# Optimization experiments

Hardware: AMD Instinct MI355X
Metric: run time of the kernel (lower is better)

Reference implementation:

```python
import jax, jax.numpy as jnp
import numpy as np

B, G1, S, GS, D, T, H = 64, 128, 32, 16, 384, 10, 6
HD = D // H
SCALE = HD ** -0.5
GELU = lambda v: jax.nn.gelu(v, approximate=False)


def layer_norm(v, g, b, eps=1e-5):
    m = jnp.mean(v, -1, keepdims=True)
    s = jnp.mean((v - m) ** 2, -1, keepdims=True)
    return (v - m) * jax.lax.rsqrt(s + eps) * g + b


def mha(xn, qkv_w, proj_w, proj_b):
    Bc, N, C = xn.shape
    qkv = (xn @ qkv_w.T).reshape(Bc, N, 3, H, HD)
    qkv = jnp.transpose(qkv, (2, 0, 3, 1, 4))  # [3,B,H,N,hd]
    q, k, v = qkv[0], qkv[1], qkv[2]
    attn = jax.nn.softmax(jnp.einsum('bhnd,bhmd->bhnm', q, k) * SCALE, axis=-1)
    o = jnp.einsum('bhnm,bhmd->bhnd', attn, v)
    o = jnp.transpose(o, (0, 2, 1, 3)).reshape(Bc, N, C)
    return o @ proj_w.T + proj_b, attn


def propagate(xyz1, xyz2, points1, points2, de_neighbors):
    # squared pairwise distances [B,N,S]
    d = jnp.sum((xyz1[:, :, None, :] - xyz2[:, None, :, :]) ** 2, -1)
    order = jnp.argsort(d, axis=-1)[..., :de_neighbors]
    dists = jnp.take_along_axis(d, order, axis=-1)
    w = 1.0 / (dists + 1e-8)
    w = w / jnp.sum(w, -1, keepdims=True)
    gathered = jax.vmap(lambda p, i: p[i])(points2, order)  # [B,N,de,Dp]
    interp = jnp.sum(gathered * w[..., None], axis=2)
    return points1 + 0.3 * interp


def setup_inputs() -> dict:
    key = jax.random.key(0)
    ks = iter(jax.random.split(key, 64))
    rn = lambda sh, sc=1.0: jax.random.normal(next(ks), sh, jnp.float32) * sc
    w = 0.02
    inp = dict(
        x=rn((B, G1 + 1, D)),
        mask=jnp.zeros((B, G1, G1), jnp.float32),
        center1=rn((B, G1, 3)),
        center2=rn((B, S, 3)),
        neighborhood=rn((B, S, GS, 3)),
        idx=jax.random.randint(next(ks), (B * S * GS,), 0, B * (G1 + T)),
        center_idx=jax.random.randint(next(ks), (B * S,), 0, B * (G1 + T)),
        group_size=GS,
        layer_id=3,
        ln1_g=jnp.ones((D,)), ln1_b=jnp.zeros((D,)),
        ln2_g=jnp.ones((D,)), ln2_b=jnp.zeros((D,)),
        qkv_w=rn((3 * D, D), w), proj_w=rn((D, D), w), proj_b=jnp.zeros((D,)),
        fc1_w=rn((4 * D, D), w), fc1_b=jnp.zeros((4 * D,)),
        fc2_w=rn((D, 4 * D), w), fc2_b=jnp.zeros((D,)),
        ad_down_w=rn((16, D), w), ad_down_b=jnp.zeros((16,)),
        ad_up_w=rn((D, 16), w), ad_up_b=jnp.zeros((D,)),
        ad1_down_w=rn((16, D), w), ad1_down_b=jnp.zeros((16,)),
        ad1_up_w=rn((D, 16), w), ad1_up_b=jnp.zeros((D,)),
        prompt_emb=rn((T, D), w),
        bn_g=jnp.ones((D,)), bn_b=jnp.zeros((D,)),
        bn_mean=jnp.zeros((D,)), bn_var=jnp.ones((D,)),
        qkv1_w=rn((3 * D, D), w), proj1_w=rn((D, D), w), proj1_b=jnp.zeros((D,)),
        ln3_g=jnp.ones((D,)), ln3_b=jnp.zeros((D,)),
    )
    return inp


def block_forward(x, mask, center1, center2, neighborhood, idx, center_idx,
                  group_size, layer_id,
                  ln1_g, ln1_b, ln2_g, ln2_b, qkv_w, proj_w, proj_b,
                  fc1_w, fc1_b, fc2_w, fc2_b,
                  ad_down_w, ad_down_b, ad_up_w, ad_up_b,
                  ad1_down_w, ad1_down_b, ad1_up_w, ad1_up_b,
                  prompt_emb, bn_g, bn_b, bn_mean, bn_var,
                  qkv1_w, proj1_w, proj1_b, ln3_g, ln3_b):
    Bc = x.shape[0]
    # mask padding (built but unused by Attention, matching the source)
    # layer_id <= 5 branch (layer_id=3)
    prompt = jnp.broadcast_to(prompt_emb[None], (Bc, T, D))  # dropout off (eval)
    x = jnp.concatenate([x[:, :1], prompt, x[:, 1:]], axis=1)  # [B, 1+T+G1, D]
    x_fn, attn_weight = mha(layer_norm(x, ln1_g, ln1_b), qkv_w, proj_w, proj_b)
    x = x_fn + x
    xn2 = layer_norm(x, ln2_g, ln2_b)
    x_fn = GELU(xn2 @ fc1_w.T + fc1_b) @ fc2_w.T + fc2_b
    # AdapterSuper_f: bottleneck down-GELU-up (no internal residual)
    ad = GELU(x_fn @ ad_down_w.T + ad_down_b) @ ad_up_w.T + ad_up_b
    x = 0.7 * ad + x_fn + x
    prompt = x[:, 1:T + 1]
    x = jnp.concatenate([x[:, :1], x[:, T + 1:]], axis=1)  # [B, 1+G1, D]
    cls_x = x[:, 0]
    x = x[:, 1:]  # [B, G1, D]
    G = G1 + T
    prompt_x = jnp.concatenate([prompt, x], axis=1).reshape(Bc * G, D)
    x_neigh = prompt_x[idx].reshape(Bc * S, group_size, D)
    x_centers = prompt_x[center_idx].reshape(Bc, S, D)
    _ = neighborhood / (jnp.std(neighborhood) + 1e-5)  # dead in source
    # local attention over each neighborhood group
    xn3 = layer_norm(x_neigh, ln3_g, ln3_b)
    attn1_out, _a = mha(xn3, qkv1_w, proj1_w, proj1_b)
    x_neigh = attn1_out + x_neigh
    # pooling: max over group, then eval BatchNorm1d + GELU over channel dim
    lc = jnp.max(x_neigh.reshape(Bc, S, group_size, D), axis=2)  # [B,S,D]
    lc = (lc - bn_mean) * jax.lax.rsqrt(bn_var + 1e-5) * bn_g + bn_b
    lc = GELU(lc)
    vis_x = lc + 0.3 * x_centers
    x = propagate(center1, center2, x, vis_x, S)
    x = jnp.concatenate([cls_x[:, None], prompt, x], axis=1)  # [B, 1+T+G1, D]
    # AdapterSuper: bottleneck with internal residual
    x = GELU(x @ ad1_down_w.T + ad1_down_b) @ ad1_up_w.T + ad1_up_b + x
    x = jnp.concatenate([x[:, :1], x[:, T + 1:]], axis=1)  # [B, 1+G1, D]
    return x, attn_weight


def reference(x, mask, center1, center2, neighborhood, idx, center_idx,
              group_size, layer_id,
              ln1_g, ln1_b, ln2_g, ln2_b, qkv_w, proj_w, proj_b,
              fc1_w, fc1_b, fc2_w, fc2_b,
              ad_down_w, ad_down_b, ad_up_w, ad_up_b,
              ad1_down_w, ad1_down_b, ad1_up_w, ad1_up_b,
              prompt_emb, bn_g, bn_b, bn_mean, bn_var,
              qkv1_w, proj1_w, proj1_b, ln3_g, ln3_b):
    return block_forward(x, mask, center1, center2, neighborhood, idx, center_idx,
                         group_size, layer_id,
                         ln1_g, ln1_b, ln2_g, ln2_b, qkv_w, proj_w, proj_b,
                         fc1_w, fc1_b, fc2_w, fc2_b,
                         ad_down_w, ad_down_b, ad_up_w, ad_up_b,
                         ad1_down_w, ad1_down_b, ad1_up_w, ad1_up_b,
                         prompt_emb, bn_g, bn_b, bn_mean, bn_var,
                         qkv1_w, proj1_w, proj1_b, ln3_g, ln3_b)
```

## Files before the change

kernel.cpp:

```cpp
#include <hip/hip_runtime.h>
#include <hip/hip_bf16.h>

typedef __hip_bfloat16 bf16;
typedef __attribute__((ext_vector_type(8))) short short8;
typedef __attribute__((ext_vector_type(4))) float f32x4;

#define DEV static __device__ __forceinline__

DEV float b2f(bf16 v) { return __bfloat162float(v); }
DEV bf16 f2b(float v) { return __float2bfloat16(v); }
DEV unsigned short f2bu(float v) { return __builtin_bit_cast(unsigned short, __float2bfloat16(v)); }
DEV float u2f(unsigned short u) { return __uint_as_float(((unsigned int)u) << 16); }
DEV float gelu(float x) { return 0.5f * x * (1.0f + erff(x * 0.70710678118654752f)); }

#define BB 64
#define NT 139
#define DD 384
#define TT 10
#define HH 6
#define GG 138
#define M1 8896
#define MG 8832
#define NGRP 2048
#define SCALE 0.125f

#define XC_OFF   0UL
#define VIS_OFF  13664256UL
#define XNB_OFF  16809984UL
#define XFN_OFF  23642112UL
#define T16_OFF  37306368UL
#define BIG1_OFF 37875712UL
#define BIG2_OFF 58372096UL
#define ATT_OFF  XNB_OFF
#define WB_OFF   85700608UL

#define WB_QKV   0
#define WB_PROJ  442368
#define WB_FC1   589824
#define WB_FC2   1179648
#define WB_QKV1  1769472
#define WB_PROJ1 2211840
#define WB_TOTAL 2359296

#define OUT_X 3170304

DEV float4 ld4(const float* p) { return *(const float4*)p; }
DEV float4 ld4(const bf16* p) {
    ushort4 u = *(const ushort4*)p;
    return make_float4(u2f(u.x), u2f(u.y), u2f(u.z), u2f(u.w));
}
DEV void stc(float* p, float v) { *p = v; }
DEV void stc(bf16* p, float v) { *p = f2b(v); }

__global__ __launch_bounds__(256) void k_wconv(const float* __restrict__ w0, const float* __restrict__ w1,
                                               const float* __restrict__ w2, const float* __restrict__ w3,
                                               const float* __restrict__ w4, const float* __restrict__ w5,
                                               bf16* __restrict__ dst) {
    int i4 = (blockIdx.x * 256 + threadIdx.x) * 4;
    if (i4 >= WB_TOTAL) return;
    const float* s; int off;
    if (i4 < WB_PROJ)       { s = w0; off = WB_QKV; }
    else if (i4 < WB_FC1)   { s = w1; off = WB_PROJ; }
    else if (i4 < WB_FC2)   { s = w2; off = WB_FC1; }
    else if (i4 < WB_QKV1)  { s = w3; off = WB_FC2; }
    else if (i4 < WB_PROJ1) { s = w4; off = WB_QKV1; }
    else                    { s = w5; off = WB_PROJ1; }
    float4 v = *(const float4*)(s + (i4 - off));
    ushort4 u;
    u.x = f2bu(v.x); u.y = f2bu(v.y); u.z = f2bu(v.z); u.w = f2bu(v.w);
    *(ushort4*)((unsigned short*)dst + i4) = u;
}

__global__ __launch_bounds__(256) void k_build_xc(const float* __restrict__ x,
                                                  const float* __restrict__ pe,
                                                  float* __restrict__ xc) {
    int i = blockIdx.x * 256 + threadIdx.x;
    if (i >= M1 * DD) return;
    int d = i % DD, r = i / DD, n = r % NT, b = r / NT;
    float v;
    if (n == 0)        v = x[(b * 129) * DD + d];
    else if (n <= TT)  v = pe[(n - 1) * DD + d];
    else               v = x[(b * 129 + n - TT) * DD + d];
    xc[i] = v;
}

__global__ __launch_bounds__(128) void k_layernorm(const float* __restrict__ src, bf16* __restrict__ dst,
                                                   const float* __restrict__ g, const float* __restrict__ bta,
                                                   int mode) {
    int r = blockIdx.x;
    int srow = r;
    if (mode) srow = (r / GG) * NT + 1 + (r % GG);
    const float* p = src + (size_t)srow * DD;
    int t = threadIdx.x;
    float v0 = p[t], v1 = p[t + 128], v2 = p[t + 256];
    __shared__ float red[4];
    float s = v0 + v1 + v2;
    for (int off = 32; off; off >>= 1) s += __shfl_down(s, off, 64);
    if ((t & 63) == 0) red[t >> 6] = s;
    __syncthreads();
    float mean = (red[0] + red[1]) * (1.0f / 384.0f);
    float d0 = v0 - mean, d1 = v1 - mean, d2 = v2 - mean;
    float s2 = d0 * d0 + d1 * d1 + d2 * d2;
    for (int off = 32; off; off >>= 1) s2 += __shfl_down(s2, off, 64);
    if ((t & 63) == 0) red[2 + (t >> 6)] = s2;
    __syncthreads();
    float rstd = rsqrtf((red[2] + red[3]) * (1.0f / 384.0f) + 1e-5f);
    bf16* q = dst + (size_t)r * DD;
    q[t]       = f2b(d0 * rstd * g[t]       + bta[t]);
    q[t + 128] = f2b(d1 * rstd * g[t + 128] + bta[t + 128]);
    q[t + 256] = f2b(d2 * rstd * g[t + 256] + bta[t + 256]);
}

template <typename TC>
__global__ __launch_bounds__(256) void mf_gemm(const bf16* __restrict__ A, const bf16* __restrict__ W,
                                               const float* __restrict__ bias, const float* __restrict__ res,
                                               TC* __restrict__ C, int M, int N, int K, int act) {
    __shared__ bf16 As[64][72];
    __shared__ bf16 Ws[64][72];
    int t = threadIdx.x;
    int m0 = blockIdx.y * 64, n0 = blockIdx.x * 64;
    int lane = t & 63, wv = t >> 6;
    int wm = (wv >> 1) * 32, wn = (wv & 1) * 32;
    int fr = lane & 15, fq = lane >> 4;
    int sr = t >> 2, sc = (t & 3) * 16;
    const bf16* pa = A + (size_t)(m0 + sr) * K + sc;
    const bf16* pw = W + (size_t)(n0 + sr) * K + sc;
    uint4 ra0 = *(const uint4*)pa;
    uint4 ra1 = *(const uint4*)(pa + 8);
    uint4 rw0 = *(const uint4*)pw;
    uint4 rw1 = *(const uint4*)(pw + 8);
    f32x4 acc[2][2] = {};
    int k0 = 0;
    for (;;) {
        *(uint4*)&As[sr][sc] = ra0; *(uint4*)&As[sr][sc + 8] = ra1;
        *(uint4*)&Ws[sr][sc] = rw0; *(uint4*)&Ws[sr][sc + 8] = rw1;
        __syncthreads();
        k0 += 64;
        bool more = (k0 < K);
        if (more) {
            ra0 = *(const uint4*)(pa + k0); ra1 = *(const uint4*)(pa + k0 + 8);
            rw0 = *(const uint4*)(pw + k0); rw1 = *(const uint4*)(pw + k0 + 8);
        }
#pragma unroll
        for (int ks = 0; ks < 2; ++ks) {
            short8 a0 = *(const short8*)&As[wm + fr][ks * 32 + fq * 8];
            short8 a1 = *(const short8*)&As[wm + 16 + fr][ks * 32 + fq * 8];
            short8 b0 = *(const short8*)&Ws[wn + fr][ks * 32 + fq * 8];
            short8 b1 = *(const short8*)&Ws[wn + 16 + fr][ks * 32 + fq * 8];
            acc[0][0] = __builtin_amdgcn_mfma_f32_16x16x32_bf16(a0, b0, acc[0][0], 0, 0, 0);
            acc[0][1] = __builtin_amdgcn_mfma_f32_16x16x32_bf16(a0, b1, acc[0][1], 0, 0, 0);
            acc[1][0] = __builtin_amdgcn_mfma_f32_16x16x32_bf16(a1, b0, acc[1][0], 0, 0, 0);
            acc[1][1] = __builtin_amdgcn_mfma_f32_16x16x32_bf16(a1, b1, acc[1][1], 0, 0, 0);
        }
        if (!more) break;
        __syncthreads();
    }
#pragma unroll
    for (int i = 0; i < 2; ++i) {
#pragma unroll
        for (int r = 0; r < 4; ++r) {
            int row = m0 + wm + i * 16 + fq * 4 + r;
            size_t ro = (size_t)row * N;
#pragma unroll
            for (int j = 0; j < 2; ++j) {
                int col = n0 + wn + j * 16 + fr;
                float c = acc[i][j][r];
                if (bias) c += bias[col];
                if (act == 1) c = gelu(c);
                if (res) c += res[ro + col];
                stc(&C[ro + col], c);
            }
        }
    }
}

#define BM 64
#define BN 64
#define BKK 16
template <typename TA, typename TC>
__global__ __launch_bounds__(256) void k_gemm(const TA* __restrict__ A, const float* __restrict__ W,
                                              const float* __restrict__ bias, const float* __restrict__ res,
                                              TC* __restrict__ C, int M, int N, int K, int act) {
    __shared__ float As[BKK][BM + 4];
    __shared__ float Wsm[BKK][BN + 4];
    int t = threadIdx.x;
    int tx = t & 15, ty = t >> 4;
    int m0 = blockIdx.y * BM, n0 = blockIdx.x * BN;
    int lr = t >> 2;
    int lk = (t & 3) * 4;
    float acc[4][4] = {};
    for (int k0 = 0; k0 < K; k0 += BKK) {
        float4 av = ld4(A + (size_t)(m0 + lr) * K + k0 + lk);
        As[lk + 0][lr] = av.x; As[lk + 1][lr] = av.y;
        As[lk + 2][lr] = av.z; As[lk + 3][lr] = av.w;
        int wrr = n0 + lr;
        float4 wv = make_float4(0.f, 0.f, 0.f, 0.f);
        if (wrr < N) wv = ld4(W + (size_t)wrr * K + k0 + lk);
        Wsm[lk + 0][lr] = wv.x; Wsm[lk + 1][lr] = wv.y;
        Wsm[lk + 2][lr] = wv.z; Wsm[lk + 3][lr] = wv.w;
        __syncthreads();
#pragma unroll
        for (int k = 0; k < BKK; ++k) {
            float a0 = As[k][ty * 4 + 0], a1 = As[k][ty * 4 + 1];
            float a2 = As[k][ty * 4 + 2], a3 = As[k][ty * 4 + 3];
            float b0 = Wsm[k][tx * 4 + 0], b1 = Wsm[k][tx * 4 + 1];
            float b2 = Wsm[k][tx * 4 + 2], b3 = Wsm[k][tx * 4 + 3];
            acc[0][0] += a0 * b0; acc[0][1] += a0 * b1; acc[0][2] += a0 * b2; acc[0][3] += a0 * b3;
            acc[1][0] += a1 * b0; acc[1][1] += a1 * b1; acc[1][2] += a1 * b2; acc[1][3] += a1 * b3;
            acc[2][0] += a2 * b0; acc[2][1] += a2 * b1; acc[2][2] += a2 * b2; acc[2][3] += a2 * b3;
            acc[3][0] += a3 * b0; acc[3][1] += a3 * b1; acc[3][2] += a3 * b2; acc[3][3] += a3 * b3;
        }
        __syncthreads();
    }
#pragma unroll
    for (int i = 0; i < 4; ++i) {
        int m = m0 + ty * 4 + i;
        size_t ro = (size_t)m * N;
#pragma unroll
        for (int j = 0; j < 4; ++j) {
            int n = n0 + tx * 4 + j;
            if (n < N) {
                float c = acc[i][j];
                if (bias) c += bias[n];
                if (act == 1) c = gelu(c);
                if (res) c += res[ro + n];
                stc(&C[ro + n], c);
            }
        }
    }
}

__global__ __launch_bounds__(256) void k_attn1(const bf16* __restrict__ qkv, bf16* __restrict__ o_out,
                                               float* __restrict__ attn_out) {
    int bh = blockIdx.x;
    int b = bh / HH, h = bh % HH;
    __shared__ unsigned short Kl[144][72];
    __shared__ unsigned short Vt[64][160];
    __shared__ unsigned short Pl[4][16][160];
    int t = threadIdx.x;
    int lane = t & 63, wv = t >> 6;
    int fr = lane & 15, fq = lane >> 4;
    const unsigned short* q16 = (const unsigned short*)qkv;
    size_t base = (size_t)b * NT * 1152;

    uint4 z4 = make_uint4(0, 0, 0, 0);
    for (int i = t * 8; i < 64 * 160; i += 2048) *(uint4*)(&Vt[0][0] + i) = z4;
    for (int i = t * 8; i < 4 * 16 * 160; i += 2048) *(uint4*)(&Pl[0][0][0] + i) = z4;
    for (int i = t; i < 144 * 8; i += 256) {
        int row = i >> 3, ch = (i & 7) * 8;
        uint4 v = z4;
        if (row < NT) v = *(const uint4*)(q16 + base + row * 1152 + 384 + h * 64 + ch);
        *(uint4*)&Kl[row][ch] = v;
    }
    for (int i = t; i < NT * 16; i += 256) {
        int m = i >> 4, dq = (i & 15) * 4;
        ushort4 v = *(const ushort4*)(q16 + base + m * 1152 + 768 + h * 64 + dq);
        Vt[dq + 0][m] = v.x; Vt[dq + 1][m] = v.y;
        Vt[dq + 2][m] = v.z; Vt[dq + 3][m] = v.w;
    }
    __syncthreads();

    for (int nt = wv; nt < 9; nt += 4) {
        int n0 = nt * 16;
        int arow = n0 + fr; if (arow > NT - 1) arow = NT - 1;
        const unsigned short* qp = q16 + base + (size_t)arow * 1152 + h * 64 + fq * 8;
        short8 a0 = *(const short8*)qp;
        short8 a1 = *(const short8*)(qp + 32);
        f32x4 s[9] = {};
#pragma unroll
        for (int mt = 0; mt < 9; ++mt) {
            short8 b0 = *(const short8*)&Kl[mt * 16 + fr][fq * 8];
            short8 b1 = *(const short8*)&Kl[mt * 16 + fr][32 + fq * 8];
            s[mt] = __builtin_amdgcn_mfma_f32_16x16x32_bf16(a0, b0, s[mt], 0, 0, 0);
            s[mt] = __builtin_amdgcn_mfma_f32_16x16x32_bf16(a1, b1, s[mt], 0, 0, 0);
        }
#pragma unroll
        for (int r = 0; r < 4; ++r) {
            float e[9];
            float mx = -1e30f;
#pragma unroll
            for (int mt = 0; mt < 9; ++mt) {
                int col = mt * 16 + fr;
                float v = (col < NT) ? s[mt][r] * SCALE : -1e30f;
                e[mt] = v;
                mx = fmaxf(mx, v);
            }
#pragma unroll
            for (int off = 1; off < 16; off <<= 1) mx = fmaxf(mx, __shfl_xor(mx, off, 64));
            float sm = 0.f;
#pragma unroll
            for (int mt = 0; mt < 9; ++mt) { e[mt] = __expf(e[mt] - mx); sm += e[mt]; }
#pragma unroll
            for (int off = 1; off < 16; off <<= 1) sm += __shfl_xor(sm, off, 64);
            float inv = 1.0f / sm;
            int n = n0 + fq * 4 + r;
            bool nv = n < NT;
            size_t ab = ((size_t)(b * HH + h) * NT + n) * NT;
#pragma unroll
            for (int mt = 0; mt < 9; ++mt) {
                float p = e[mt] * inv;
                int col = mt * 16 + fr;
                if (nv && col < NT) attn_out[ab + col] = p;
                Pl[wv][fq * 4 + r][col] = f2bu(p);
            }
        }
        __syncthreads();
        f32x4 oac[4] = {};
#pragma unroll
        for (int ks = 0; ks < 5; ++ks) {
            short8 ap = *(const short8*)&Pl[wv][fr][ks * 32 + fq * 8];
#pragma unroll
            for (int dt = 0; dt < 4; ++dt) {
                short8 bv = *(const short8*)&Vt[dt * 16 + fr][ks * 32 + fq * 8];
                oac[dt] = __builtin_amdgcn_mfma_f32_16x16x32_bf16(ap, bv, oac[dt], 0, 0, 0);
            }
        }
#pragma unroll
        for (int dt = 0; dt < 4; ++dt)
#pragma unroll
            for (int r = 0; r < 4; ++r) {
                int n = n0 + fq * 4 + r;
                if (n < NT)
                    o_out[((size_t)(b * NT + n)) * DD + h * 64 + dt * 16 + fr] = f2b(oac[dt][r]);
            }
    }
}

__global__ __launch_bounds__(64) void k_attn2(const bf16* __restrict__ qkv, const int* __restrict__ idx,
                                              bf16* __restrict__ o1) {
    int g = blockIdx.x;
    __shared__ unsigned short Vt2[64][40];
    __shared__ unsigned short P2[16][40];
    __shared__ int ridx[16];
    int t = threadIdx.x;
    int fr = t & 15, fq = t >> 4;
    const unsigned short* q16 = (const unsigned short*)qkv;
    if (t < 16) ridx[t] = idx[g * 16 + t];
    uint4 z4 = make_uint4(0, 0, 0, 0);
    for (int i = t * 8; i < 64 * 40; i += 512) *(uint4*)(&Vt2[0][0] + i) = z4;
    for (int i = t * 8; i < 16 * 40; i += 512) *(uint4*)(&P2[0][0] + i) = z4;
    __syncthreads();
    size_t qb = (size_t)ridx[fr] * 1152;
    for (int h = 0; h < HH; ++h) {
        for (int i = t; i < 256; i += 64) {
            int m = i >> 4, dq = (i & 15) * 4;
            ushort4 v = *(const ushort4*)(q16 + (size_t)ridx[m] * 1152 + 768 + h * 64 + dq);
            Vt2[dq + 0][m] = v.x; Vt2[dq + 1][m] = v.y;
            Vt2[dq + 2][m] = v.z; Vt2[dq + 3][m] = v.w;
        }
        __syncthreads();
        const unsigned short* qp = q16 + qb + h * 64 + fq * 8;
        const unsigned short* kp = q16 + qb + 384 + h * 64 + fq * 8;
        short8 a0 = *(const short8*)qp;
        short8 a1 = *(const short8*)(qp + 32);
        short8 b0 = *(const short8*)kp;
        short8 b1 = *(const short8*)(kp + 32);
        f32x4 s = {};
        s = __builtin_amdgcn_mfma_f32_16x16x32_bf16(a0, b0, s, 0, 0, 0);
        s = __builtin_amdgcn_mfma_f32_16x16x32_bf16(a1, b1, s, 0, 0, 0);
#pragma unroll
        for (int r = 0; r < 4; ++r) {
            float v = s[r] * SCALE;
            float mx = v;
#pragma unroll
            for (int off = 1; off < 16; off <<= 1) mx = fmaxf(mx, __shfl_xor(mx, off, 64));
            float e = __expf(v - mx), sm = e;
#pragma unroll
            for (int off = 1; off < 16; off <<= 1) sm += __shfl_xor(sm, off, 64);
            P2[fq * 4 + r][fr] = f2bu(e / sm);
        }
        __syncthreads();
        short8 ap = *(const short8*)&P2[fr][fq * 8];
        f32x4 oac[4] = {};
#pragma unroll
        for (int dt = 0; dt < 4; ++dt) {
            short8 bv = *(const short8*)&Vt2[dt * 16 + fr][fq * 8];
            oac[dt] = __builtin_amdgcn_mfma_f32_16x16x32_bf16(ap, bv, oac[dt], 0, 0, 0);
        }
#pragma unroll
        for (int dt = 0; dt < 4; ++dt)
#pragma unroll
            for (int r = 0; r < 4; ++r)
                o1[((size_t)(g * 16 + fq * 4 + r)) * DD + h * 64 + dt * 16 + fr] = f2b(oac[dt][r]);
        __syncthreads();
    }
}

__global__ __launch_bounds__(128) void k_ad_combine(const float* __restrict__ t16, const float* __restrict__ upw,
                                                    const float* __restrict__ upb, const float* __restrict__ xfn,
                                                    float* xc) {
    int r = blockIdx.x, t = threadIdx.x;
    __shared__ float tl[16];
    if (t < 16) tl[t] = t16[r * 16 + t];
    __syncthreads();
    for (int d = t; d < DD; d += 128) {
        float acc = 0.f;
#pragma unroll
        for (int c = 0; c < 4; ++c) {
            float4 u = *(const float4*)(upw + d * 16 + c * 4);
            acc += tl[c * 4 + 0] * u.x + tl[c * 4 + 1] * u.y
                 + tl[c * 4 + 2] * u.z + tl[c * 4 + 3] * u.w;
        }
        acc += upb[d];
        size_t i = (size_t)r * DD + d;
        xc[i] += 0.7f * acc + xfn[i];
    }
}

__global__ __launch_bounds__(128) void k_groupmax(const bf16* __restrict__ att, const float* __restrict__ xc,
                                                  const int* __restrict__ idx, const int* __restrict__ cidx,
                                                  const float* __restrict__ bg, const float* __restrict__ bb,
                                                  const float* __restrict__ bmean, const float* __restrict__ bvar,
                                                  float* __restrict__ vis) {
    int g = blockIdx.x, t = threadIdx.x;
    __shared__ int rows[16];
    __shared__ int crow;
    if (t < 16) { int r = idx[g * 16 + t]; rows[t] = (r / GG) * NT + 1 + (r % GG); }
    if (t == 16) { int r = cidx[g]; crow = (r / GG) * NT + 1 + (r % GG); }
    __syncthreads();
    for (int d = t; d < DD; d += 128) {
        float m = -INFINITY;
#pragma unroll
        for (int j = 0; j < 16; ++j) {
            float v = b2f(att[((size_t)(g * 16 + j)) * DD + d]) + xc[(size_t)rows[j] * DD + d];
            m = fmaxf(m, v);
        }
        float bn = (m - bmean[d]) * rsqrtf(bvar[d] + 1e-5f) * bg[d] + bb[d];
        bn = gelu(bn);
        vis[(size_t)g * DD + d] = bn + 0.3f * xc[(size_t)crow * DD + d];
    }
}

__global__ __launch_bounds__(128) void k_propagate(const float* __restrict__ c1, const float* __restrict__ c2,
                                                   const float* __restrict__ xc, const float* __restrict__ vis,
                                                   float* __restrict__ xp) {
    int blk = blockIdx.x;
    int b = blk >> 7, i = blk & 127;
    int t = threadIdx.x;
    __shared__ float wl[32];
    __shared__ float wsum;
    if (t < 32) {
        float dx = c1[(b * 128 + i) * 3 + 0] - c2[(b * 32 + t) * 3 + 0];
        float dy = c1[(b * 128 + i) * 3 + 1] - c2[(b * 32 + t) * 3 + 1];
        float dz = c1[(b * 128 + i) * 3 + 2] - c2[(b * 32 + t) * 3 + 2];
        wl[t] = 1.0f / (dx * dx + dy * dy + dz * dz + 1e-8f);
    }
    __syncthreads();
    if (t == 0) {
        float s = 0.f;
        for (int j = 0; j < 32; ++j) s += wl[j];
        wsum = s;
    }
    __syncthreads();
    float sc = 0.3f / wsum;
    for (int d = t; d < DD; d += 128) {
        float acc = 0.f;
#pragma unroll 8
        for (int j = 0; j < 32; ++j) acc += wl[j] * vis[((size_t)(b * 32 + j)) * DD + d];
        xp[((size_t)(b * 128 + i)) * DD + d] = xc[((size_t)(b * NT + 11 + i)) * DD + d] + sc * acc;
    }
}

__global__ __launch_bounds__(256) void k_build_xfinal(const float* __restrict__ xc, const float* __restrict__ xp,
                                                      float* __restrict__ xf) {
    int i = blockIdx.x * 256 + threadIdx.x;
    if (i >= M1 * DD) return;
    int d = i % DD, r = i / DD, n = r % NT, b = r / NT;
    xf[i] = (n < 11) ? xc[i] : xp[((size_t)(b * 128 + n - 11)) * DD + d];
}

__global__ __launch_bounds__(128) void k_final(const float* __restrict__ t16, const float* __restrict__ upw,
                                               const float* __restrict__ upb, const float* __restrict__ xf,
                                               float* __restrict__ outx) {
    int rb = blockIdx.x, t = threadIdx.x;
    int b = rb / 129, no = rb % 129;
    int src = b * NT + (no == 0 ? 0 : no + TT);
    __shared__ float tl[16];
    if (t < 16) tl[t] = t16[src * 16 + t];
    __syncthreads();
    for (int d = t; d < DD; d += 128) {
        float acc = 0.f;
#pragma unroll
        for (int c = 0; c < 4; ++c) {
            float4 u = *(const float4*)(upw + d * 16 + c * 4);
            acc += tl[c * 4 + 0] * u.x + tl[c * 4 + 1] * u.y
                 + tl[c * 4 + 2] * u.z + tl[c * 4 + 3] * u.w;
        }
        acc += upb[d];
        outx[(size_t)rb * DD + d] = acc + xf[(size_t)src * DD + d];
    }
}

extern "C" void kernel_launch(void* const* d_in, const int* in_sizes, int n_in,
                              void* d_out, int out_size, void* d_ws, size_t ws_size,
                              hipStream_t stream) {
    const float* x_in    = (const float*)d_in[0];
    const float* center1 = (const float*)d_in[2];
    const float* center2 = (const float*)d_in[3];
    const int*   idx     = (const int*)d_in[5];
    const int*   cidx    = (const int*)d_in[6];
    const float* ln1_g   = (const float*)d_in[9];
    const float* ln1_b   = (const float*)d_in[10];
    const float* ln2_g   = (const float*)d_in[11];
    const float* ln2_b   = (const float*)d_in[12];
    const float* qkv_w   = (const float*)d_in[13];
    const float* proj_w  = (const float*)d_in[14];
    const float* proj_b  = (const float*)d_in[15];
    const float* fc1_w   = (const float*)d_in[16];
    const float* fc1_b   = (const float*)d_in[17];
    const float* fc2_w   = (const float*)d_in[18];
    const float* fc2_b   = (const float*)d_in[19];
    const float* ad_dw   = (const float*)d_in[20];
    const float* ad_db   = (const float*)d_in[21];
    const float* ad_uw   = (const float*)d_in[22];
    const float* ad_ub   = (const float*)d_in[23];
    const float* ad1_dw  = (const float*)d_in[24];
    const float* ad1_db  = (const float*)d_in[25];
    const float* ad1_uw  = (const float*)d_in[26];
    const float* ad1_ub  = (const float*)d_in[27];
    const float* prompt  = (const float*)d_in[28];
    const float* bn_g    = (const float*)d_in[29];
    const float* bn_b    = (const float*)d_in[30];
    const float* bn_mean = (const float*)d_in[31];
    const float* bn_var  = (const float*)d_in[32];
    const float* qkv1_w  = (const float*)d_in[33];
    const float* proj1_w = (const float*)d_in[34];
    const float* proj1_b = (const float*)d_in[35];
    const float* ln3_g   = (const float*)d_in[36];
    const float* ln3_b   = (const float*)d_in[37];

    char* wsb = (char*)d_ws;
    float* XC   = (float*)(wsb + XC_OFF);
    float* VIS  = (float*)(wsb + VIS_OFF);
    bf16*  XNB  = (bf16*)(wsb + XNB_OFF);
    float* XFN  = (float*)(wsb + XFN_OFF);
    float* T16  = (float*)(wsb + T16_OFF);
    bf16*  BIG1 = (bf16*)(wsb + BIG1_OFF);
    bf16*  BIG2 = (bf16*)(wsb + BIG2_OFF);
    float* XFIN = (float*)(wsb + BIG2_OFF);
    bf16*  ATT  = (bf16*)(wsb + ATT_OFF);
    bf16*  WB   = (bf16*)(wsb + WB_OFF);

    float* out_x    = (float*)d_out;
    float* out_attn = out_x + OUT_X;

    k_wconv<<<(WB_TOTAL / 4 + 255) / 256, 256, 0, stream>>>(qkv_w, proj_w, fc1_w, fc2_w, qkv1_w, proj1_w, WB);

    k_build_xc<<<(M1 * DD + 255) / 256, 256, 0, stream>>>(x_in, prompt, XC);
    k_layernorm<<<M1, 128, 0, stream>>>(XC, XNB, ln1_g, ln1_b, 0);
    mf_gemm<<<dim3(18, 139), 256, 0, stream>>>(XNB, WB + WB_QKV, (const float*)nullptr, (const float*)nullptr, BIG1, M1, 1152, 384, 0);
    k_attn1<<<BB * HH, 256, 0, stream>>>(BIG1, XNB, out_attn);
    mf_gemm<<<dim3(6, 139), 256, 0, stream>>>(XNB, WB + WB_PROJ, proj_b, XC, XC, M1, 384, 384, 0);
    k_layernorm<<<M1, 128, 0, stream>>>(XC, XNB, ln2_g, ln2_b, 0);
    mf_gemm<<<dim3(24, 139), 256, 0, stream>>>(XNB, WB + WB_FC1, fc1_b, (const float*)nullptr, BIG2, M1, 1536, 384, 1);
    mf_gemm<<<dim3(6, 139), 256, 0, stream>>>(BIG2, WB + WB_FC2, fc2_b, (const float*)nullptr, XFN, M1, 384, 1536, 0);
    k_gemm<<<dim3(1, 139), 256, 0, stream>>>(XFN, ad_dw, ad_db, (const float*)nullptr, T16, M1, 16, 384, 1);
    k_ad_combine<<<M1, 128, 0, stream>>>(T16, ad_uw, ad_ub, XFN, XC);

    k_layernorm<<<MG, 128, 0, stream>>>(XC, XNB, ln3_g, ln3_b, 1);
    mf_gemm<<<dim3(18, 138), 256, 0, stream>>>(XNB, WB + WB_QKV1, (const float*)nullptr, (const float*)nullptr, BIG1, MG, 1152, 384, 0);
    k_attn2<<<NGRP, 64, 0, stream>>>(BIG1, idx, BIG2);
    mf_gemm<<<dim3(6, 512), 256, 0, stream>>>(BIG2, WB + WB_PROJ1, proj1_b, (const float*)nullptr, ATT, NGRP * 16, 384, 384, 0);
    k_groupmax<<<NGRP, 128, 0, stream>>>(ATT, XC, idx, cidx, bn_g, bn_b, bn_mean, bn_var, VIS);
    k_propagate<<<BB * 128, 128, 0, stream>>>(center1, center2, XC, VIS, XFN);

    k_build_xfinal<<<(M1 * DD + 255) / 256, 256, 0, stream>>>(XC, XFN, XFIN);
    k_gemm<<<dim3(1, 139), 256, 0, stream>>>(XFIN, ad1_dw, ad1_db, (const float*)nullptr, T16, M1, 16, 384, 1);
    k_final<<<BB * 129, 128, 0, stream>>>(T16, ad1_uw, ad1_ub, XFIN, out_x);
}
```

Measured before the change: 503.0 us.

## Enlarge MFMA GEMM tiles to 128x128 with direct global-to-LDS loads

```diff
diff --git a/kernel.cpp b/kernel.cpp
--- a/kernel.cpp
+++ b/kernel.cpp
@@ -12,6 +12,11 @@
 DEV unsigned short f2bu(float v) { return __builtin_bit_cast(unsigned short, __float2bfloat16(v)); }
 DEV float u2f(unsigned short u) { return __uint_as_float(((unsigned int)u) << 16); }
 DEV float gelu(float x) { return 0.5f * x * (1.0f + erff(x * 0.70710678118654752f)); }
+
+DEV void gld16(bf16* lds, const bf16* g) {
+    __builtin_amdgcn_global_load_lds((__attribute__((address_space(1))) void*)g,
+                                     (__attribute__((address_space(3))) void*)lds, 16, 0, 0);
+}
 
 #define BB 64
 #define NT 139
@@ -115,60 +120,60 @@
 __global__ __launch_bounds__(256) void mf_gemm(const bf16* __restrict__ A, const bf16* __restrict__ W,
                                                const float* __restrict__ bias, const float* __restrict__ res,
                                                TC* __restrict__ C, int M, int N, int K, int act) {
-    __shared__ bf16 As[64][72];
-    __shared__ bf16 Ws[64][72];
+    __shared__ bf16 As[128 * 64];
+    __shared__ bf16 Ws[128 * 64];
     int t = threadIdx.x;
-    int m0 = blockIdx.y * 64, n0 = blockIdx.x * 64;
     int lane = t & 63, wv = t >> 6;
-    int wm = (wv >> 1) * 32, wn = (wv & 1) * 32;
+    int m0 = blockIdx.y * 128, n0 = blockIdx.x * 128;
+    int wm = (wv >> 1) * 64, wn = (wv & 1) * 64;
     int fr = lane & 15, fq = lane >> 4;
-    int sr = t >> 2, sc = (t & 3) * 16;
-    const bf16* pa = A + (size_t)(m0 + sr) * K + sc;
-    const bf16* pw = W + (size_t)(n0 + sr) * K + sc;
-    uint4 ra0 = *(const uint4*)pa;
-    uint4 ra1 = *(const uint4*)(pa + 8);
-    uint4 rw0 = *(const uint4*)pw;
-    uint4 rw1 = *(const uint4*)(pw + 8);
-    f32x4 acc[2][2] = {};
-    int k0 = 0;
-    for (;;) {
-        *(uint4*)&As[sr][sc] = ra0; *(uint4*)&As[sr][sc + 8] = ra1;
-        *(uint4*)&Ws[sr][sc] = rw0; *(uint4*)&Ws[sr][sc + 8] = rw1;
-        __syncthreads();
-        k0 += 64;
-        bool more = (k0 < K);
-        if (more) {
-            ra0 = *(const uint4*)(pa + k0); ra1 = *(const uint4*)(pa + k0 + 8);
-            rw0 = *(const uint4*)(pw + k0); rw1 = *(const uint4*)(pw + k0 + 8);
-        }
+    int srow = wv * 32 + (lane >> 3);
+    int scol = (lane & 7) * 8;
+    const bf16* pa = A + (size_t)(m0 + srow) * K + scol;
+    const bf16* pw = W + (size_t)(n0 + srow) * K + scol;
+    bf16* la = As + wv * 2048;
+    bf16* lw = Ws + wv * 2048;
+    f32x4 acc[4][4] = {};
+    for (int k0 = 0; k0 < K; k0 += 64) {
+#pragma unroll
+        for (int i = 0; i < 4; ++i) {
+            gld16(la + i * 512, pa + (size_t)(i * 8) * K + k0);
+            gld16(lw + i * 512, pw + (size_t)(i * 8) * K + k0);
+        }
+        __syncthreads();
 #pragma unroll
         for (int ks = 0; ks < 2; ++ks) {
-            short8 a0 = *(const short8*)&As[wm + fr][ks * 32 + fq * 8];
-            short8 a1 = *(const short8*)&As[wm + 16 + fr][ks * 32 + fq * 8];
-            short8 b0 = *(const short8*)&Ws[wn + fr][ks * 32 + fq * 8];
-            short8 b1 = *(const short8*)&Ws[wn + 16 + fr][ks * 32 + fq * 8];
-            acc[0][0] = __builtin_amdgcn_mfma_f32_16x16x32_bf16(a0, b0, acc[0][0], 0, 0, 0);
-            acc[0][1] = __builtin_amdgcn_mfma_f32_16x16x32_bf16(a0, b1, acc[0][1], 0, 0, 0);
-            acc[1][0] = __builtin_amdgcn_mfma_f32_16x16x32_bf16(a1, b0, acc[1][0], 0, 0, 0);
-            acc[1][1] = __builtin_amdgcn_mfma_f32_16x16x32_bf16(a1, b1, acc[1][1], 0, 0, 0);
-        }
-        if (!more) break;
-        __syncthreads();
-    }
-#pragma unroll
-    for (int i = 0; i < 2; ++i) {
+            short8 a[4], b[4];
+#pragma unroll
+            for (int mi = 0; mi < 4; ++mi)
+                a[mi] = *(const short8*)&As[(wm + mi * 16 + fr) * 64 + ks * 32 + fq * 8];
+#pragma unroll
+            for (int ni = 0; ni < 4; ++ni)
+                b[ni] = *(const short8*)&Ws[(wn + ni * 16 + fr) * 64 + ks * 32 + fq * 8];
+#pragma unroll
+            for (int mi = 0; mi < 4; ++mi)
+#pragma unroll
+                for (int ni = 0; ni < 4; ++ni)
+                    acc[mi][ni] = __builtin_amdgcn_mfma_f32_16x16x32_bf16(a[mi], b[ni], acc[mi][ni], 0, 0, 0);
+        }
+        __syncthreads();
+    }
+#pragma unroll
+    for (int mi = 0; mi < 4; ++mi) {
 #pragma unroll
         for (int r = 0; r < 4; ++r) {
-            int row = m0 + wm + i * 16 + fq * 4 + r;
-            size_t ro = (size_t)row * N;
-#pragma unroll
-            for (int j = 0; j < 2; ++j) {
-                int col = n0 + wn + j * 16 + fr;
-                float c = acc[i][j][r];
-                if (bias) c += bias[col];
-                if (act == 1) c = gelu(c);
-                if (res) c += res[ro + col];
-                stc(&C[ro + col], c);
+            int row = m0 + wm + mi * 16 + fq * 4 + r;
+            if (row < M) {
+                size_t ro = (size_t)row * N;
+#pragma unroll
+                for (int ni = 0; ni < 4; ++ni) {
+                    int col = n0 + wn + ni * 16 + fr;
+                    float c = acc[mi][ni][r];
+                    if (bias) c += bias[col];
+                    if (act == 1) c = gelu(c);
+                    if (res) c += res[ro + col];
+                    stc(&C[ro + col], c);
+                }
             }
         }
     }
@@ -548,19 +553,19 @@
 
     k_build_xc<<<(M1 * DD + 255) / 256, 256, 0, stream>>>(x_in, prompt, XC);
     k_layernorm<<<M1, 128, 0, stream>>>(XC, XNB, ln1_g, ln1_b, 0);
-    mf_gemm<<<dim3(18, 139), 256, 0, stream>>>(XNB, WB + WB_QKV, (const float*)nullptr, (const float*)nullptr, BIG1, M1, 1152, 384, 0);
+    mf_gemm<<<dim3(9, 70), 256, 0, stream>>>(XNB, WB + WB_QKV, (const float*)nullptr, (const float*)nullptr, BIG1, M1, 1152, 384, 0);
     k_attn1<<<BB * HH, 256, 0, stream>>>(BIG1, XNB, out_attn);
-    mf_gemm<<<dim3(6, 139), 256, 0, stream>>>(XNB, WB + WB_PROJ, proj_b, XC, XC, M1, 384, 384, 0);
+    mf_gemm<<<dim3(3, 70), 256, 0, stream>>>(XNB, WB + WB_PROJ, proj_b, XC, XC, M1, 384, 384, 0);
     k_layernorm<<<M1, 128, 0, stream>>>(XC, XNB, ln2_g, ln2_b, 0);
-    mf_gemm<<<dim3(24, 139), 256, 0, stream>>>(XNB, WB + WB_FC1, fc1_b, (const float*)nullptr, BIG2, M1, 1536, 384, 1);
-    mf_gemm<<<dim3(6, 139), 256, 0, stream>>>(BIG2, WB + WB_FC2, fc2_b, (const float*)nullptr, XFN, M1, 384, 1536, 0);
+    mf_gemm<<<dim3(12, 70), 256, 0, stream>>>(XNB, WB + WB_FC1, fc1_b, (const float*)nullptr, BIG2, M1, 1536, 384, 1);
+    mf_gemm<<<dim3(3, 70), 256, 0, stream>>>(BIG2, WB + WB_FC2, fc2_b, (const float*)nullptr, XFN, M1, 384, 1536, 0);
     k_gemm<<<dim3(1, 139), 256, 0, stream>>>(XFN, ad_dw, ad_db, (const float*)nullptr, T16, M1, 16, 384, 1);
     k_ad_combine<<<M1, 128, 0, stream>>>(T16, ad_uw, ad_ub, XFN, XC);
 
     k_layernorm<<<MG, 128, 0, stream>>>(XC, XNB, ln3_g, ln3_b, 1);
-    mf_gemm<<<dim3(18, 138), 256, 0, stream>>>(XNB, WB + WB_QKV1, (const float*)nullptr, (const float*)nullptr, BIG1, MG, 1152, 384, 0);
+    mf_gemm<<<dim3(9, 69), 256, 0, stream>>>(XNB, WB + WB_QKV1, (const float*)nullptr, (const float*)nullptr, BIG1, MG, 1152, 384, 0);
     k_attn2<<<NGRP, 64, 0, stream>>>(BIG1, idx, BIG2);
-    mf_gemm<<<dim3(6, 512), 256, 0, stream>>>(BIG2, WB + WB_PROJ1, proj1_b, (const float*)nullptr, ATT, NGRP * 16, 384, 384, 0);
+    mf_gemm<<<dim3(3, 256), 256, 0, stream>>>(BIG2, WB + WB_PROJ1, proj1_b, (const float*)nullptr, ATT, NGRP * 16, 384, 384, 0);
     k_groupmax<<<NGRP, 128, 0, stream>>>(ATT, XC, idx, cidx, bn_g, bn_b, bn_mean, bn_var, VIS);
     k_propagate<<<BB * 128, 128, 0, stream>>>(center1, center2, XC, VIS, XFN);
 
```

Result: slower. 591.2 us (+17.5%).

## Fuse input build with layernorm and adapter down/up projections into single kernels

Applied to the files above, without the earlier changes.

```diff
diff --git a/kernel.cpp b/kernel.cpp
--- a/kernel.cpp
+++ b/kernel.cpp
@@ -71,17 +71,35 @@
     *(ushort4*)((unsigned short*)dst + i4) = u;
 }
 
-__global__ __launch_bounds__(256) void k_build_xc(const float* __restrict__ x,
-                                                  const float* __restrict__ pe,
-                                                  float* __restrict__ xc) {
-    int i = blockIdx.x * 256 + threadIdx.x;
-    if (i >= M1 * DD) return;
-    int d = i % DD, r = i / DD, n = r % NT, b = r / NT;
-    float v;
-    if (n == 0)        v = x[(b * 129) * DD + d];
-    else if (n <= TT)  v = pe[(n - 1) * DD + d];
-    else               v = x[(b * 129 + n - TT) * DD + d];
-    xc[i] = v;
+__global__ __launch_bounds__(128) void k_build_ln(const float* __restrict__ x, const float* __restrict__ pe,
+                                                  const float* __restrict__ g, const float* __restrict__ bta,
+                                                  float* __restrict__ xc, bf16* __restrict__ dst) {
+    int r = blockIdx.x;
+    int n = r % NT, b = r / NT;
+    const float* p;
+    if (n == 0)       p = x + (size_t)(b * 129) * DD;
+    else if (n <= TT) p = pe + (size_t)(n - 1) * DD;
+    else              p = x + (size_t)(b * 129 + n - TT) * DD;
+    int t = threadIdx.x;
+    float v0 = p[t], v1 = p[t + 128], v2 = p[t + 256];
+    float* xr = xc + (size_t)r * DD;
+    xr[t] = v0; xr[t + 128] = v1; xr[t + 256] = v2;
+    __shared__ float red[4];
+    float s = v0 + v1 + v2;
+    for (int off = 32; off; off >>= 1) s += __shfl_down(s, off, 64);
+    if ((t & 63) == 0) red[t >> 6] = s;
+    __syncthreads();
+    float mean = (red[0] + red[1]) * (1.0f / 384.0f);
+    float d0 = v0 - mean, d1 = v1 - mean, d2 = v2 - mean;
+    float s2 = d0 * d0 + d1 * d1 + d2 * d2;
+    for (int off = 32; off; off >>= 1) s2 += __shfl_down(s2, off, 64);
+    if ((t & 63) == 0) red[2 + (t >> 6)] = s2;
+    __syncthreads();
+    float rstd = rsqrtf((red[2] + red[3]) * (1.0f / 384.0f) + 1e-5f);
+    bf16* q = dst + (size_t)r * DD;
+    q[t]       = f2b(d0 * rstd * g[t]       + bta[t]);
+    q[t + 128] = f2b(d1 * rstd * g[t + 128] + bta[t + 128]);
+    q[t + 256] = f2b(d2 * rstd * g[t + 256] + bta[t + 256]);
 }
 
 __global__ __launch_bounds__(128) void k_layernorm(const float* __restrict__ src, bf16* __restrict__ dst,
@@ -174,59 +192,49 @@
     }
 }
 
-#define BM 64
-#define BN 64
-#define BKK 16
-template <typename TA, typename TC>
-__global__ __launch_bounds__(256) void k_gemm(const TA* __restrict__ A, const float* __restrict__ W,
-                                              const float* __restrict__ bias, const float* __restrict__ res,
-                                              TC* __restrict__ C, int M, int N, int K, int act) {
-    __shared__ float As[BKK][BM + 4];
-    __shared__ float Wsm[BKK][BN + 4];
-    int t = threadIdx.x;
-    int tx = t & 15, ty = t >> 4;
-    int m0 = blockIdx.y * BM, n0 = blockIdx.x * BN;
-    int lr = t >> 2;
-    int lk = (t & 3) * 4;
-    float acc[4][4] = {};
-    for (int k0 = 0; k0 < K; k0 += BKK) {
-        float4 av = ld4(A + (size_t)(m0 + lr) * K + k0 + lk);
-        As[lk + 0][lr] = av.x; As[lk + 1][lr] = av.y;
-        As[lk + 2][lr] = av.z; As[lk + 3][lr] = av.w;
-        int wrr = n0 + lr;
-        float4 wv = make_float4(0.f, 0.f, 0.f, 0.f);
-        if (wrr < N) wv = ld4(W + (size_t)wrr * K + k0 + lk);
-        Wsm[lk + 0][lr] = wv.x; Wsm[lk + 1][lr] = wv.y;
-        Wsm[lk + 2][lr] = wv.z; Wsm[lk + 3][lr] = wv.w;
-        __syncthreads();
-#pragma unroll
-        for (int k = 0; k < BKK; ++k) {
-            float a0 = As[k][ty * 4 + 0], a1 = As[k][ty * 4 + 1];
-            float a2 = As[k][ty * 4 + 2], a3 = As[k][ty * 4 + 3];
-            float b0 = Wsm[k][tx * 4 + 0], b1 = Wsm[k][tx * 4 + 1];
-            float b2 = Wsm[k][tx * 4 + 2], b3 = Wsm[k][tx * 4 + 3];
-            acc[0][0] += a0 * b0; acc[0][1] += a0 * b1; acc[0][2] += a0 * b2; acc[0][3] += a0 * b3;
-            acc[1][0] += a1 * b0; acc[1][1] += a1 * b1; acc[1][2] += a1 * b2; acc[1][3] += a1 * b3;
-            acc[2][0] += a2 * b0; acc[2][1] += a2 * b1; acc[2][2] += a2 * b2; acc[2][3] += a2 * b3;
-            acc[3][0] += a3 * b0; acc[3][1] += a3 * b1; acc[3][2] += a3 * b2; acc[3][3] += a3 * b3;
-        }
-        __syncthreads();
-    }
-#pragma unroll
-    for (int i = 0; i < 4; ++i) {
-        int m = m0 + ty * 4 + i;
-        size_t ro = (size_t)m * N;
-#pragma unroll
-        for (int j = 0; j < 4; ++j) {
-            int n = n0 + tx * 4 + j;
-            if (n < N) {
-                float c = acc[i][j];
-                if (bias) c += bias[n];
-                if (act == 1) c = gelu(c);
-                if (res) c += res[ro + n];
-                stc(&C[ro + n], c);
-            }
-        }
+__global__ __launch_bounds__(128) void k_adapter(const float* __restrict__ srcbuf,
+                                                 const float* __restrict__ dw, const float* __restrict__ db,
+                                                 const float* __restrict__ uw, const float* __restrict__ ub,
+                                                 float* __restrict__ dst, int mode) {
+    int rb = blockIdx.x, t = threadIdx.x;
+    const float* s;
+    float* d;
+    if (mode == 0) {
+        s = srcbuf + (size_t)rb * DD;
+        d = dst + (size_t)rb * DD;
+    } else {
+        int b = rb / 129, no = rb % 129;
+        int srow = b * NT + (no == 0 ? 0 : no + TT);
+        s = srcbuf + (size_t)srow * DD;
+        d = dst + (size_t)rb * DD;
+    }
+    __shared__ float tl[16];
+    int g = t >> 3, sub = t & 7;
+    const float* wg = dw + g * DD + sub * 48;
+    const float* sg = s + sub * 48;
+    float part = 0.f;
+#pragma unroll
+    for (int j = 0; j < 12; ++j) {
+        float4 a = *(const float4*)(sg + j * 4);
+        float4 w = *(const float4*)(wg + j * 4);
+        part += a.x * w.x + a.y * w.y + a.z * w.z + a.w * w.w;
+    }
+    part += __shfl_xor(part, 1, 64);
+    part += __shfl_xor(part, 2, 64);
+    part += __shfl_xor(part, 4, 64);
+    if (sub == 0) tl[g] = gelu(part + db[g]);
+    __syncthreads();
+    for (int dd = t; dd < DD; dd += 128) {
+        float acc = 0.f;
+#pragma unroll
+        for (int c = 0; c < 4; ++c) {
+            float4 u = *(const float4*)(uw + dd * 16 + c * 4);
+            acc += tl[c * 4 + 0] * u.x + tl[c * 4 + 1] * u.y
+                 + tl[c * 4 + 2] * u.z + tl[c * 4 + 3] * u.w;
+        }
+        acc += ub[dd];
+        if (mode == 0) d[dd] += 0.7f * acc + s[dd];
+        else           d[dd] = acc + s[dd];
     }
 }
 
@@ -386,27 +394,6 @@
     }
 }
 
-__global__ __launch_bounds__(128) void k_ad_combine(const float* __restrict__ t16, const float* __restrict__ upw,
-                                                    const float* __restrict__ upb, const float* __restrict__ xfn,
-                                                    float* xc) {
-    int r = blockIdx.x, t = threadIdx.x;
-    __shared__ float tl[16];
-    if (t < 16) tl[t] = t16[r * 16 + t];
-    __syncthreads();
-    for (int d = t; d < DD; d += 128) {
-        float acc = 0.f;
-#pragma unroll
-        for (int c = 0; c < 4; ++c) {
-            float4 u = *(const float4*)(upw + d * 16 + c * 4);
-            acc += tl[c * 4 + 0] * u.x + tl[c * 4 + 1] * u.y
-                 + tl[c * 4 + 2] * u.z + tl[c * 4 + 3] * u.w;
-        }
-        acc += upb[d];
-        size_t i = (size_t)r * DD + d;
-        xc[i] += 0.7f * acc + xfn[i];
-    }
-}
-
 __global__ __launch_bounds__(128) void k_groupmax(const bf16* __restrict__ att, const float* __restrict__ xc,
                                                   const int* __restrict__ idx, const int* __restrict__ cidx,
                                                   const float* __restrict__ bg, const float* __restrict__ bb,
@@ -467,28 +454,6 @@
     if (i >= M1 * DD) return;
     int d = i % DD, r = i / DD, n = r % NT, b = r / NT;
     xf[i] = (n < 11) ? xc[i] : xp[((size_t)(b * 128 + n - 11)) * DD + d];
-}
-
-__global__ __launch_bounds__(128) void k_final(const float* __restrict__ t16, const float* __restrict__ upw,
-                                               const float* __restrict__ upb, const float* __restrict__ xf,
-                                               float* __restrict__ outx) {
-    int rb = blockIdx.x, t = threadIdx.x;
-    int b = rb / 129, no = rb % 129;
-    int src = b * NT + (no == 0 ? 0 : no + TT);
-    __shared__ float tl[16];
-    if (t < 16) tl[t] = t16[src * 16 + t];
-    __syncthreads();
-    for (int d = t; d < DD; d += 128) {
-        float acc = 0.f;
-#pragma unroll
-        for (int c = 0; c < 4; ++c) {
-            float4 u = *(const float4*)(upw + d * 16 + c * 4);
-            acc += tl[c * 4 + 0] * u.x + tl[c * 4 + 1] * u.y
-                 + tl[c * 4 + 2] * u.z + tl[c * 4 + 3] * u.w;
-        }
-        acc += upb[d];
-        outx[(size_t)rb * DD + d] = acc + xf[(size_t)src * DD + d];
-    }
 }
 
 extern "C" void kernel_launch(void* const* d_in, const int* in_sizes, int n_in,
@@ -534,7 +499,6 @@
     float* VIS  = (float*)(wsb + VIS_OFF);
     bf16*  XNB  = (bf16*)(wsb + XNB_OFF);
     float* XFN  = (float*)(wsb + XFN_OFF);
-    float* T16  = (float*)(wsb + T16_OFF);
     bf16*  BIG1 = (bf16*)(wsb + BIG1_OFF);
     bf16*  BIG2 = (bf16*)(wsb + BIG2_OFF);
     float* XFIN = (float*)(wsb + BIG2_OFF);
@@ -546,16 +510,14 @@
 
     k_wconv<<<(WB_TOTAL / 4 + 255) / 256, 256, 0, stream>>>(qkv_w, proj_w, fc1_w, fc2_w, qkv1_w, proj1_w, WB);
 
-    k_build_xc<<<(M1 * DD + 255) / 256, 256, 0, stream>>>(x_in, prompt, XC);
-    k_layernorm<<<M1, 128, 0, stream>>>(XC, XNB, ln1_g, ln1_b, 0);
+    k_build_ln<<<M1, 128, 0, stream>>>(x_in, prompt, ln1_g, ln1_b, XC, XNB);
     mf_gemm<<<dim3(18, 139), 256, 0, stream>>>(XNB, WB + WB_QKV, (const float*)nullptr, (const float*)nullptr, BIG1, M1, 1152, 384, 0);
     k_attn1<<<BB * HH, 256, 0, stream>>>(BIG1, XNB, out_attn);
     mf_gemm<<<dim3(6, 139), 256, 0, stream>>>(XNB, WB + WB_PROJ, proj_b, XC, XC, M1, 384, 384, 0);
     k_layernorm<<<M1, 128, 0, stream>>>(XC, XNB, ln2_g, ln2_b, 0);
     mf_gemm<<<dim3(24, 139), 256, 0, stream>>>(XNB, WB + WB_FC1, fc1_b, (const float*)nullptr, BIG2, M1, 1536, 384, 1);
     mf_gemm<<<dim3(6, 139), 256, 0, stream>>>(BIG2, WB + WB_FC2, fc2_b, (const float*)nullptr, XFN, M1, 384, 1536, 0);
-    k_gemm<<<dim3(1, 139), 256, 0, stream>>>(XFN, ad_dw, ad_db, (const float*)nullptr, T16, M1, 16, 384, 1);
-    k_ad_combine<<<M1, 128, 0, stream>>>(T16, ad_uw, ad_ub, XFN, XC);
+    k_adapter<<<M1, 128, 0, stream>>>(XFN, ad_dw, ad_db, ad_uw, ad_ub, XC, 0);
 
     k_layernorm<<<MG, 128, 0, stream>>>(XC, XNB, ln3_g, ln3_b, 1);
     mf_gemm<<<dim3(18, 138), 256, 0, stream>>>(XNB, WB + WB_QKV1, (const float*)nullptr, (const float*)nullptr, BIG1, MG, 1152, 384, 0);
@@ -565,6 +527,5 @@
     k_propagate<<<BB * 128, 128, 0, stream>>>(center1, center2, XC, VIS, XFN);
 
     k_build_xfinal<<<(M1 * DD + 255) / 256, 256, 0, stream>>>(XC, XFN, XFIN);
-    k_gemm<<<dim3(1, 139), 256, 0, stream>>>(XFIN, ad1_dw, ad1_db, (const float*)nullptr, T16, M1, 16, 384, 1);
-    k_final<<<BB * 129, 128, 0, stream>>>(T16, ad1_uw, ad1_ub, XFIN, out_x);
-}
+    k_adapter<<<BB * 129, 128, 0, stream>>>(XFIN, ad1_dw, ad1_db, ad1_uw, ad1_ub, out_x, 1);
+}
```

Result: faster. 492.2 us (-2.1%).
